# Kernel tuning notes

Measured on AMD Instinct MI355X. Metric: run time of the kernel, lower is better.

The kernel has to match this reference:

```python
import jax, jax.numpy as jnp
import numpy as np

N = 100000                       # all_nodes_num
COUNTS = (40000, 30000, 30000)   # node_type_split_list; type 0 is the attributed type
HID = 64                         # args.hidden_dim
K = 8                            # args.cluster_num
E = 1_600_000                    # number of edges in g
D_IN = 512                       # in_dims[valid_attributed_type]
NCLS = 16                        # num_classes


def _spmm_mean(h, src, dst):
    """Degree-normalized sparse adjacency @ h via gather/segment_sum (edge-list spmm)."""
    deg = jax.ops.segment_sum(jnp.ones_like(src, dtype=h.dtype), dst, num_segments=N)
    agg = jax.ops.segment_sum(h[src], dst, num_segments=N)  # [N, HID]
    return agg / jnp.maximum(deg, 1.0)[:, None]


def setup_inputs() -> dict:
    key = jax.random.key(0)
    ks = jax.random.split(key, 16)
    s = lambda k, shp, fan: jax.random.normal(k, shp, jnp.float32) * np.float32(1.0 / np.sqrt(fan))
    return {
        "feats0": jax.random.normal(ks[0], (COUNTS[0], D_IN), jnp.float32),
        "W_pre": s(ks[1], (D_IN, HID), D_IN), "b_pre": jnp.zeros((HID,), jnp.float32),
        "emb_W": s(ks[2], (2, COUNTS[1], HID), COUNTS[1]), "emb_b": jnp.zeros((2, HID), jnp.float32),
        "op_W": s(ks[3], (K, HID, HID), HID), "op_b": jnp.zeros((K, HID), jnp.float32),
        "fc_W": s(ks[4], (2, HID, HID), HID), "fc_b": jnp.zeros((2, HID), jnp.float32),
        "gnn_W": s(ks[5], (HID, HID), HID), "gnn_b": jnp.zeros((HID,), jnp.float32),
        "out_W": s(ks[6], (HID, NCLS), HID), "out_b": jnp.zeros((NCLS,), jnp.float32),
        "src": jax.random.randint(ks[7], (E,), 0, N, jnp.int32),
        "dst": jax.random.randint(ks[8], (E,), 0, N, jnp.int32),
        "node_assign": jax.random.randint(ks[9], (N,), 0, K, jnp.int32),
    }


def reference(feats0, W_pre, b_pre, emb_W, emb_b, op_W, op_b, fc_W, fc_b,
              gnn_W, gnn_b, out_W, out_b, src, dst, node_assign):
    # preprocess: Linear on the attributed type, scattered into h0 over all nodes
    h_attr = feats0 @ W_pre + b_pre                       # [n0, HID]
    h0 = jnp.zeros((N, HID), feats0.dtype).at[:COUNTS[0]].set(h_attr)

    # 'one-hot' embeddings: Linear applied to sparse identity == weight rows + bias
    one_hot_h = jnp.concatenate([
        jnp.zeros((COUNTS[0], HID), feats0.dtype),
        emb_W[0] + emb_b[0],
        emb_W[1] + emb_b[1],
    ], axis=0)                                            # [N, HID]

    # shared heterogeneous-graph aggregation (edge-list spmm), per-cluster op linear,
    # then diagonal cluster mask (spmm with diagonal selection matrix == row masking)
    agg = _spmm_mean(h0, src, dst)                        # [N, HID]
    h_att = h0
    for k in range(K):
        mask = (node_assign == k)[:, None]
        gcn_k = agg @ op_W[k] + op_b[k]                   # per-cluster GNN op output
        h_att = h_att + jnp.where(mask, gcn_k + one_hot_h, 0.0)

    # useTypeLinear: per-type Linear for non-attributed types, identity for attributed
    parts = [h_att[:COUNTS[0]]]
    off = COUNTS[0]
    for i in range(2):
        seg = h_att[off:off + COUNTS[1 + i]]
        parts.append(seg @ fc_W[i] + fc_b[i])
        off += COUNTS[1 + i]
    h_t = jnp.concatenate(parts, axis=0)                  # [N, HID]

    # downstream GCN-style model: spmm -> linear -> elu, then classifier head
    node_emb = jax.nn.elu(_spmm_mean(h_t, src, dst) @ gnn_W + gnn_b)
    logits = node_emb @ out_W + out_b
    return node_emb, logits, logits
```

## Files before the change

kernel.cpp:

```cpp
#include <hip/hip_runtime.h>
#include <hip/hip_bf16.h>

#define NN   100000
#define C0   40000
#define C1   30000
#define C2   30000
#define HID  64
#define KK   8
#define EE   1600000
#define DIN  512
#define NCLS 16
#define NB   196
#define BKE  2048
#define GR1  782
#define PMB  625
#define NBC  1568
#define SCH  7
#define MAXT 1571
#define FCT  469
#define GNT  1563
#define AP   88

typedef unsigned short ushortT;
typedef __attribute__((ext_vector_type(8))) short bf16x8;
typedef __attribute__((ext_vector_type(4))) float f32x4;

__device__ __forceinline__ float b2f(ushortT u) {
    return __uint_as_float((unsigned)u << 16);
}
__device__ __forceinline__ ushortT f2b(float x) {
    unsigned v = __float_as_uint(x);
    unsigned r = (v + 0x7FFF + ((v >> 16) & 1)) >> 16;
    return (ushortT)r;
}
__device__ __forceinline__ unsigned pk2(float lo, float hi) {
    return (unsigned)f2b(lo) | ((unsigned)f2b(hi) << 16);
}
__device__ __forceinline__ void acc8f(float* a, uint4 v) {
    a[0] += b2f((ushortT)(v.x & 0xFFFF)); a[1] += b2f((ushortT)(v.x >> 16));
    a[2] += b2f((ushortT)(v.y & 0xFFFF)); a[3] += b2f((ushortT)(v.y >> 16));
    a[4] += b2f((ushortT)(v.z & 0xFFFF)); a[5] += b2f((ushortT)(v.z >> 16));
    a[6] += b2f((ushortT)(v.w & 0xFFFF)); a[7] += b2f((ushortT)(v.w >> 16));
}

__global__ __launch_bounds__(256) void zero_wt(const float* __restrict__ W,
                                               ushortT* __restrict__ WT,
                                               int* __restrict__ bcnt) {
    const int t = threadIdx.x, b = blockIdx.x;
    if (b < 16) {
        int idx = b * 256 + t;
        int c = idx >> 6, k8 = (idx & 63) * 8;
        uint4 v;
        v.x = pk2(W[(size_t)(k8 + 0) * HID + c], W[(size_t)(k8 + 1) * HID + c]);
        v.y = pk2(W[(size_t)(k8 + 2) * HID + c], W[(size_t)(k8 + 3) * HID + c]);
        v.z = pk2(W[(size_t)(k8 + 4) * HID + c], W[(size_t)(k8 + 5) * HID + c]);
        v.w = pk2(W[(size_t)(k8 + 6) * HID + c], W[(size_t)(k8 + 7) * HID + c]);
        *(uint4*)(WT + (size_t)c * DIN + k8) = v;
    } else {
        if (t < NB) bcnt[t] = 0;
    }
}

__global__ __launch_bounds__(256) void fused_a(const float* __restrict__ A,
                                               const ushortT* __restrict__ WT,
                                               const float* __restrict__ bias,
                                               const int* __restrict__ dst,
                                               const int* __restrict__ na,
                                               int* __restrict__ bcnt,
                                               int* __restrict__ nbc,
                                               ushortT* __restrict__ hb) {
    __shared__ ushortT Ak[2][64 * AP];
    __shared__ ushortT Bk[2][64 * AP];
    const int tid = threadIdx.x, b = blockIdx.x;
    if (b < PMB) {
        const int row0 = b * 64;
        const int rr = tid >> 2, q = tid & 3;
        const int w = tid >> 6, l = tid & 63;
        const int lr = l & 15, g = l >> 4;
        f32x4 acc[4] = {{0.f,0.f,0.f,0.f},{0.f,0.f,0.f,0.f},{0.f,0.f,0.f,0.f},{0.f,0.f,0.f,0.f}};
        float4 av0, av1, av2, av3;
        uint4 bv0, bv1;
        {
            const float* ap = A + (size_t)(row0 + rr) * DIN + q * 16;
            av0 = *(const float4*)(ap + 0);  av1 = *(const float4*)(ap + 4);
            av2 = *(const float4*)(ap + 8);  av3 = *(const float4*)(ap + 12);
            const uint4* bp = (const uint4*)(WT + (size_t)rr * DIN + q * 16);
            bv0 = bp[0]; bv1 = bp[1];
        }
        {
            uint4 ua0, ua1;
            ua0.x = pk2(av0.x, av0.y); ua0.y = pk2(av0.z, av0.w);
            ua0.z = pk2(av1.x, av1.y); ua0.w = pk2(av1.z, av1.w);
            ua1.x = pk2(av2.x, av2.y); ua1.y = pk2(av2.z, av2.w);
            ua1.z = pk2(av3.x, av3.y); ua1.w = pk2(av3.z, av3.w);
            *(uint4*)&Ak[0][rr * AP + q * 16] = ua0;
            *(uint4*)&Ak[0][rr * AP + q * 16 + 8] = ua1;
            *(uint4*)&Bk[0][rr * AP + q * 16] = bv0;
            *(uint4*)&Bk[0][rr * AP + q * 16 + 8] = bv1;
        }
        __syncthreads();
        for (int tt = 0; tt < 8; ++tt) {
            if (tt < 7) {
                const int k0 = (tt + 1) * 64;
                const float* ap = A + (size_t)(row0 + rr) * DIN + k0 + q * 16;
                av0 = *(const float4*)(ap + 0);  av1 = *(const float4*)(ap + 4);
                av2 = *(const float4*)(ap + 8);  av3 = *(const float4*)(ap + 12);
                const uint4* bp = (const uint4*)(WT + (size_t)rr * DIN + k0 + q * 16);
                bv0 = bp[0]; bv1 = bp[1];
            }
            const int bu = tt & 1;
            #pragma unroll
            for (int s = 0; s < 2; ++s) {
                bf16x8 af = *(const bf16x8*)&Ak[bu][(w * 16 + lr) * AP + s * 32 + g * 8];
                #pragma unroll
                for (int n = 0; n < 4; ++n) {
                    bf16x8 bf = *(const bf16x8*)&Bk[bu][(n * 16 + lr) * AP + s * 32 + g * 8];
                    acc[n] = __builtin_amdgcn_mfma_f32_16x16x32_bf16(af, bf, acc[n], 0, 0, 0);
                }
            }
            if (tt < 7) {
                const int nb2 = (tt + 1) & 1;
                uint4 ua0, ua1;
                ua0.x = pk2(av0.x, av0.y); ua0.y = pk2(av0.z, av0.w);
                ua0.z = pk2(av1.x, av1.y); ua0.w = pk2(av1.z, av1.w);
                ua1.x = pk2(av2.x, av2.y); ua1.y = pk2(av2.z, av2.w);
                ua1.z = pk2(av3.x, av3.y); ua1.w = pk2(av3.z, av3.w);
                *(uint4*)&Ak[nb2][rr * AP + q * 16] = ua0;
                *(uint4*)&Ak[nb2][rr * AP + q * 16 + 8] = ua1;
                *(uint4*)&Bk[nb2][rr * AP + q * 16] = bv0;
                *(uint4*)&Bk[nb2][rr * AP + q * 16 + 8] = bv1;
            }
            __syncthreads();
        }
        #pragma unroll
        for (int n = 0; n < 4; ++n) {
            float bb = bias[n * 16 + lr];
            #pragma unroll
            for (int i = 0; i < 4; ++i) {
                int row = row0 + w * 16 + g * 4 + i;
                hb[(size_t)row * HID + n * 16 + lr] = f2b(acc[n][i] + bb);
            }
        }
    } else if (b < PMB + GR1) {
        int* sh = (int*)&Ak[0][0];
        for (int i = tid; i < NB; i += 256) sh[i] = 0;
        __syncthreads();
        const int base = (b - PMB) * BKE;
        for (int u = 0; u < BKE / 256; ++u) {
            int e = base + tid + u * 256;
            if (e < EE) atomicAdd(&sh[dst[e] >> 9], 1);
        }
        __syncthreads();
        for (int i = tid; i < NB; i += 256) {
            int c = sh[i];
            if (c) atomicAdd(&bcnt[i], c);
        }
    } else {
        int* sh = (int*)&Ak[0][0];
        const int nb_ = b - PMB - GR1;
        if (tid < KK) sh[tid] = 0;
        __syncthreads();
        #pragma unroll
        for (int u = 0; u < 2; ++u) {
            int n = nb_ * 512 + tid + u * 256;
            if (n < NN) atomicAdd(&sh[na[n]], 1);
        }
        __syncthreads();
        if (tid < KK) nbc[tid * NB + nb_] = sh[tid];
    }
}

__global__ __launch_bounds__(256) void scan_k(const int* __restrict__ bcnt,
                                              int* __restrict__ bbase,
                                              int* __restrict__ bcur,
                                              int* __restrict__ offs,
                                              const int* __restrict__ nbc,
                                              int* __restrict__ gbase,
                                              int* __restrict__ koff,
                                              int* __restrict__ tmap_b,
                                              int* __restrict__ tmap_s) {
    __shared__ int sm[256];
    const int t = threadIdx.x;
    if (blockIdx.x == 0) {
        int v = (t < NB) ? bcnt[t] : 0;
        sm[t] = v;
        __syncthreads();
        for (int off = 1; off < 256; off <<= 1) {
            int y = (t >= off) ? sm[t - off] : 0;
            __syncthreads();
            sm[t] += y;
            __syncthreads();
        }
        if (t < NB) {
            int excl = sm[t] - v;
            bbase[t] = excl;
            bcur[t] = excl;
        }
        if (t == 0) offs[NN] = EE;
        return;
    }
    __shared__ int carry;
    __shared__ int tl[KK];
    if (t == 0) carry = 0;
    for (int i = t; i < MAXT; i += 256) tmap_b[i] = -1;
    __syncthreads();
    for (int c = 0; c < SCH; ++c) {
        int i = c * 256 + t;
        int v = (i < NBC) ? nbc[i] : 0;
        sm[t] = v;
        __syncthreads();
        for (int off = 1; off < 256; off <<= 1) {
            int y = (t >= off) ? sm[t - off] : 0;
            __syncthreads();
            sm[t] += y;
            __syncthreads();
        }
        int base = carry;
        int excl = base + sm[t] - v;
        if (i < NBC) {
            gbase[i] = excl;
            if ((i % NB) == 0) koff[i / NB] = excl;
        }
        __syncthreads();
        if (t == 255) carry = base + sm[255];
        __syncthreads();
    }
    if (t == 0) {
        koff[KK] = NN;
        int run = 0;
        for (int k = 0; k < KK; ++k) {
            tl[k] = run;
            int cnt = ((k == KK - 1) ? NN : koff[k + 1]) - koff[k];
            run += (cnt + 63) / 64;
        }
    }
    __syncthreads();
    if (t < KK) {
        int k = t;
        int kb = koff[k];
        int ke = (k == KK - 1) ? NN : koff[k + 1];
        int nt = (ke - kb + 63) / 64;
        for (int tt = 0; tt < nt; ++tt) {
            tmap_b[tl[k] + tt] = k;
            tmap_s[tl[k] + tt] = kb + tt * 64;
        }
    }
}

__global__ __launch_bounds__(256) void scatter_k(const int* __restrict__ src,
                                                 const int* __restrict__ dst,
                                                 int* __restrict__ bcur,
                                                 unsigned* __restrict__ ebuf,
                                                 const int* __restrict__ na,
                                                 const int* __restrict__ gbase,
                                                 int* __restrict__ perm) {
    __shared__ int s1[NB];
    __shared__ int s2[NB];
    const int t = threadIdx.x, b = blockIdx.x;
    if (b < GR1) {
        for (int i = t; i < NB; i += 256) s1[i] = 0;
        __syncthreads();
        const int base = b * BKE;
        unsigned mypk[8]; int mybin[8], myrank[8];
        #pragma unroll
        for (int u = 0; u < 8; ++u) {
            int e = base + t + u * 256;
            if (e < EE) {
                int d = dst[e];
                int s = src[e];
                mybin[u] = d >> 9;
                mypk[u] = (unsigned)s |
                          ((unsigned)(((d & 511) << 1) | (s < C0 ? 0 : 1)) << 17);
                myrank[u] = atomicAdd(&s1[mybin[u]], 1);
            } else mybin[u] = -1;
        }
        __syncthreads();
        for (int i = t; i < NB; i += 256) {
            int c = s1[i];
            s2[i] = c ? atomicAdd(&bcur[i], c) : 0;
        }
        __syncthreads();
        #pragma unroll
        for (int u = 0; u < 8; ++u) {
            if (mybin[u] >= 0) {
                ebuf[s2[mybin[u]] + myrank[u]] = mypk[u];
            }
        }
    } else {
        const int nb_ = b - GR1;
        if (t < KK) { s1[t] = 0; s2[t] = gbase[t * NB + nb_]; }
        __syncthreads();
        #pragma unroll
        for (int u = 0; u < 2; ++u) {
            int n = nb_ * 512 + t + u * 256;
            if (n < NN) {
                int k = na[n];
                int r = atomicAdd(&s1[k], 1);
                perm[s2[k] + r] = n;
            }
        }
    }
}

__global__ __launch_bounds__(256) void fine_scatter(const unsigned* __restrict__ ebuf,
                                                    const int* __restrict__ bbase,
                                                    const int* __restrict__ bend,
                                                    int* __restrict__ offs,
                                                    int* __restrict__ split,
                                                    int* __restrict__ ssrc) {
    __shared__ int hist[1024];
    __shared__ int lofs[1024];
    __shared__ int sm[256];
    const int t = threadIdx.x, b = blockIdx.x;
    const int beg = bbase[b], end = bend[b];
    for (int i = t; i < 1024; i += 256) hist[i] = 0;
    __syncthreads();
    for (int j = beg + t; j < end; j += 256) {
        unsigned pk = ebuf[j];
        atomicAdd(&hist[pk >> 17], 1);
    }
    __syncthreads();
    int v0 = hist[4 * t], v1 = hist[4 * t + 1], v2 = hist[4 * t + 2], v3 = hist[4 * t + 3];
    int ts = v0 + v1 + v2 + v3;
    sm[t] = ts;
    __syncthreads();
    for (int off = 1; off < 256; off <<= 1) {
        int y = (t >= off) ? sm[t - off] : 0;
        __syncthreads();
        sm[t] += y;
        __syncthreads();
    }
    int pre = sm[t] - ts;
    lofs[4 * t] = pre; lofs[4 * t + 1] = pre + v0;
    lofs[4 * t + 2] = pre + v0 + v1; lofs[4 * t + 3] = pre + v0 + v1 + v2;
    __syncthreads();
    const int d0 = b * 512;
    for (int i = t; i < 512; i += 256) {
        int n = d0 + i;
        if (n < NN) {
            offs[n]  = beg + lofs[2 * i];
            split[n] = beg + lofs[2 * i + 1];
        }
    }
    __syncthreads();
    for (int j = beg + t; j < end; j += 256) {
        unsigned pk = ebuf[j];
        int pos = beg + atomicAdd(&lofs[pk >> 17], 1);
        ssrc[pos] = (int)(pk & 0x1FFFFu);
    }
}

__global__ __launch_bounds__(256) void spmm(const ushortT* __restrict__ rows,
                                            const int* __restrict__ offs,
                                            const int* __restrict__ splt,
                                            const int* __restrict__ ssrc,
                                            ushortT* __restrict__ aggb) {
    const int t = threadIdx.x;
    const int g = t >> 3, c8 = t & 7;
    const int n = blockIdx.x * 32 + g;
    const int beg = offs[n], endf = offs[n + 1];
    const int ge = splt ? splt[n] : endf;
    float a[8] = {}, c[8] = {};
    int j = beg;
    for (; j + 8 <= ge; j += 8) {
        int s0 = ssrc[j + 0], s1 = ssrc[j + 1], s2 = ssrc[j + 2], s3 = ssrc[j + 3];
        int s4 = ssrc[j + 4], s5 = ssrc[j + 5], s6 = ssrc[j + 6], s7 = ssrc[j + 7];
        uint4 v0 = *(const uint4*)(rows + (size_t)s0 * HID + c8 * 8);
        uint4 v1 = *(const uint4*)(rows + (size_t)s1 * HID + c8 * 8);
        uint4 v2 = *(const uint4*)(rows + (size_t)s2 * HID + c8 * 8);
        uint4 v3 = *(const uint4*)(rows + (size_t)s3 * HID + c8 * 8);
        uint4 v4 = *(const uint4*)(rows + (size_t)s4 * HID + c8 * 8);
        uint4 v5 = *(const uint4*)(rows + (size_t)s5 * HID + c8 * 8);
        uint4 v6 = *(const uint4*)(rows + (size_t)s6 * HID + c8 * 8);
        uint4 v7 = *(const uint4*)(rows + (size_t)s7 * HID + c8 * 8);
        acc8f(a, v0); acc8f(c, v1); acc8f(a, v2); acc8f(c, v3);
        acc8f(a, v4); acc8f(c, v5); acc8f(a, v6); acc8f(c, v7);
    }
    if (j + 4 <= ge) {
        int s0 = ssrc[j + 0], s1 = ssrc[j + 1], s2 = ssrc[j + 2], s3 = ssrc[j + 3];
        uint4 v0 = *(const uint4*)(rows + (size_t)s0 * HID + c8 * 8);
        uint4 v1 = *(const uint4*)(rows + (size_t)s1 * HID + c8 * 8);
        uint4 v2 = *(const uint4*)(rows + (size_t)s2 * HID + c8 * 8);
        uint4 v3 = *(const uint4*)(rows + (size_t)s3 * HID + c8 * 8);
        acc8f(a, v0); acc8f(c, v1); acc8f(a, v2); acc8f(c, v3);
        j += 4;
    }
    for (; j < ge; ++j) {
        uint4 v = *(const uint4*)(rows + (size_t)ssrc[j] * HID + c8 * 8);
        acc8f(a, v);
    }
    const float inv = 1.0f / fmaxf((float)(endf - beg), 1.0f);
    #pragma unroll
    for (int i = 0; i < 8; ++i) a[i] = (a[i] + c[i]) * inv;
    uint4 o;
    o.x = pk2(a[0], a[1]); o.y = pk2(a[2], a[3]);
    o.z = pk2(a[4], a[5]); o.w = pk2(a[6], a[7]);
    *(uint4*)(aggb + (size_t)n * HID + c8 * 8) = o;
}

__device__ __forceinline__ void gemm64(const float As[64][65], const float Bs[64][64],
                                       float acc[4][4], int tx, int ty) {
    for (int kk = 0; kk < 64; ++kk) {
        float a0 = As[ty * 4 + 0][kk], a1 = As[ty * 4 + 1][kk];
        float a2 = As[ty * 4 + 2][kk], a3 = As[ty * 4 + 3][kk];
        float4 bv = *(const float4*)(&Bs[kk][tx * 4]);
        acc[0][0] += a0 * bv.x; acc[0][1] += a0 * bv.y; acc[0][2] += a0 * bv.z; acc[0][3] += a0 * bv.w;
        acc[1][0] += a1 * bv.x; acc[1][1] += a1 * bv.y; acc[1][2] += a1 * bv.z; acc[1][3] += a1 * bv.w;
        acc[2][0] += a2 * bv.x; acc[2][1] += a2 * bv.y; acc[2][2] += a2 * bv.z; acc[2][3] += a2 * bv.w;
        acc[3][0] += a3 * bv.x; acc[3][1] += a3 * bv.y; acc[3][2] += a3 * bv.z; acc[3][3] += a3 * bv.w;
    }
}

__global__ __launch_bounds__(256) void op_gemm(const ushortT* __restrict__ aggb,
                                               const ushortT* __restrict__ hb,
                                               const int* __restrict__ perm,
                                               const int* __restrict__ koff,
                                               const int* __restrict__ tmap_b,
                                               const int* __restrict__ tmap_s,
                                               const float* __restrict__ op_W,
                                               const float* __restrict__ op_b,
                                               const float* __restrict__ emb_W,
                                               const float* __restrict__ emb_b,
                                               ushortT* __restrict__ htb) {
    __shared__ float As[64][65];
    __shared__ float Bs[64][64];
    __shared__ int idx[64];
    const int bk = tmap_b[blockIdx.x];
    if (bk < 0) return;
    const int start = tmap_s[blockIdx.x];
    const int kend = koff[bk + 1];
    const int tid = threadIdx.x;
    if (tid < 64) {
        int p = start + tid;
        idx[tid] = (p < kend) ? perm[p] : -1;
    }
    __syncthreads();
    for (int i = tid; i < 64 * 16; i += 256) {
        int r = i >> 4, c4 = i & 15;
        int n = idx[r];
        if (n >= 0) {
            ushort4 u = *(const ushort4*)(aggb + (size_t)n * HID + c4 * 4);
            As[r][c4 * 4 + 0] = b2f(u.x); As[r][c4 * 4 + 1] = b2f(u.y);
            As[r][c4 * 4 + 2] = b2f(u.z); As[r][c4 * 4 + 3] = b2f(u.w);
        } else {
            As[r][c4 * 4 + 0] = 0.f; As[r][c4 * 4 + 1] = 0.f;
            As[r][c4 * 4 + 2] = 0.f; As[r][c4 * 4 + 3] = 0.f;
        }
    }
    for (int i = tid; i < 64 * 16; i += 256) {
        int r = i >> 4, c4 = i & 15;
        *(float4*)(&Bs[r][c4 * 4]) = *(const float4*)(op_W + (size_t)bk * HID * HID + (size_t)r * HID + c4 * 4);
    }
    __syncthreads();
    const int tx = tid & 15, ty = tid >> 4;
    float acc[4][4] = {};
    gemm64(As, Bs, acc, tx, ty);
    float4 ob = *(const float4*)(op_b + (size_t)bk * HID + tx * 4);
    #pragma unroll
    for (int rr = 0; rr < 4; ++rr) {
        int n = idx[ty * 4 + rr];
        if (n < 0) continue;
        float4 v;
        v.x = acc[rr][0] + ob.x; v.y = acc[rr][1] + ob.y;
        v.z = acc[rr][2] + ob.z; v.w = acc[rr][3] + ob.w;
        if (n < C0) {
            ushort4 hu = *(const ushort4*)(hb + (size_t)n * HID + tx * 4);
            v.x += b2f(hu.x); v.y += b2f(hu.y); v.z += b2f(hu.z); v.w += b2f(hu.w);
        } else {
            int si = (n < C0 + C1) ? 0 : 1;
            int rn = n - C0 - si * C1;
            float4 ew = *(const float4*)(emb_W + ((size_t)si * C1 + rn) * HID + tx * 4);
            float4 eb = *(const float4*)(emb_b + (size_t)si * HID + tx * 4);
            v.x += ew.x + eb.x; v.y += ew.y + eb.y;
            v.z += ew.z + eb.z; v.w += ew.w + eb.w;
        }
        ushort4 o;
        o.x = f2b(v.x); o.y = f2b(v.y); o.z = f2b(v.z); o.w = f2b(v.w);
        *(ushort4*)(htb + (size_t)n * HID + tx * 4) = o;
    }
}

__global__ __launch_bounds__(256) void fc_gemm(ushortT* __restrict__ htb,
                                               const float* __restrict__ fc_W,
                                               const float* __restrict__ fc_b) {
    __shared__ float As[64][65];
    __shared__ float Bs[64][64];
    const int si = (blockIdx.x < FCT) ? 0 : 1;
    const int t0 = blockIdx.x - si * FCT;
    const int row0 = C0 + si * C1 + t0 * 64;
    const int lim = C0 + (si + 1) * C1;
    const int tid = threadIdx.x;
    for (int i = tid; i < 64 * 16; i += 256) {
        int r = i >> 4, c4 = i & 15;
        int n = row0 + r;
        if (n < lim) {
            ushort4 u = *(const ushort4*)(htb + (size_t)n * HID + c4 * 4);
            As[r][c4 * 4 + 0] = b2f(u.x); As[r][c4 * 4 + 1] = b2f(u.y);
            As[r][c4 * 4 + 2] = b2f(u.z); As[r][c4 * 4 + 3] = b2f(u.w);
        } else {
            As[r][c4 * 4 + 0] = 0.f; As[r][c4 * 4 + 1] = 0.f;
            As[r][c4 * 4 + 2] = 0.f; As[r][c4 * 4 + 3] = 0.f;
        }
    }
    for (int i = tid; i < 64 * 16; i += 256) {
        int r = i >> 4, c4 = i & 15;
        *(float4*)(&Bs[r][c4 * 4]) = *(const float4*)(fc_W + (size_t)si * HID * HID + (size_t)r * HID + c4 * 4);
    }
    __syncthreads();
    const int tx = tid & 15, ty = tid >> 4;
    float acc[4][4] = {};
    gemm64(As, Bs, acc, tx, ty);
    float4 fb = *(const float4*)(fc_b + (size_t)si * HID + tx * 4);
    #pragma unroll
    for (int rr = 0; rr < 4; ++rr) {
        int n = row0 + ty * 4 + rr;
        if (n >= lim) continue;
        ushort4 o;
        o.x = f2b(acc[rr][0] + fb.x); o.y = f2b(acc[rr][1] + fb.y);
        o.z = f2b(acc[rr][2] + fb.z); o.w = f2b(acc[rr][3] + fb.w);
        *(ushort4*)(htb + (size_t)n * HID + tx * 4) = o;
    }
}

__global__ __launch_bounds__(256) void gnn_logits(const ushortT* __restrict__ aggb,
                                                  const float* __restrict__ gnn_W,
                                                  const float* __restrict__ gnn_b,
                                                  const float* __restrict__ out_W,
                                                  const float* __restrict__ out_b,
                                                  float* __restrict__ out) {
    __shared__ float As[64][65];
    __shared__ float Bs[64][64];
    __shared__ float Wo[64 * NCLS];
    const int row0 = blockIdx.x * 64;
    const int tid = threadIdx.x;
    for (int i = tid; i < 64 * 16; i += 256) {
        int r = i >> 4, c4 = i & 15;
        int n = row0 + r;
        if (n < NN) {
            ushort4 u = *(const ushort4*)(aggb + (size_t)n * HID + c4 * 4);
            As[r][c4 * 4 + 0] = b2f(u.x); As[r][c4 * 4 + 1] = b2f(u.y);
            As[r][c4 * 4 + 2] = b2f(u.z); As[r][c4 * 4 + 3] = b2f(u.w);
        } else {
            As[r][c4 * 4 + 0] = 0.f; As[r][c4 * 4 + 1] = 0.f;
            As[r][c4 * 4 + 2] = 0.f; As[r][c4 * 4 + 3] = 0.f;
        }
    }
    for (int i = tid; i < 64 * 16; i += 256) {
        int r = i >> 4, c4 = i & 15;
        *(float4*)(&Bs[r][c4 * 4]) = *(const float4*)(gnn_W + (size_t)r * HID + c4 * 4);
    }
    *(float4*)(&Wo[tid * 4]) = *(const float4*)(out_W + tid * 4);
    __syncthreads();
    const int tx = tid & 15, ty = tid >> 4;
    float acc[4][4] = {};
    gemm64(As, Bs, acc, tx, ty);
    __syncthreads();
    float4 gb = *(const float4*)(gnn_b + tx * 4);
    #pragma unroll
    for (int rr = 0; rr < 4; ++rr) {
        int n = row0 + ty * 4 + rr;
        float4 v;
        v.x = acc[rr][0] + gb.x; v.y = acc[rr][1] + gb.y;
        v.z = acc[rr][2] + gb.z; v.w = acc[rr][3] + gb.w;
        v.x = (v.x > 0.f) ? v.x : expm1f(v.x);
        v.y = (v.y > 0.f) ? v.y : expm1f(v.y);
        v.z = (v.z > 0.f) ? v.z : expm1f(v.z);
        v.w = (v.w > 0.f) ? v.w : expm1f(v.w);
        As[ty * 4 + rr][tx * 4 + 0] = v.x; As[ty * 4 + rr][tx * 4 + 1] = v.y;
        As[ty * 4 + rr][tx * 4 + 2] = v.z; As[ty * 4 + rr][tx * 4 + 3] = v.w;
        if (n < NN) *(float4*)(out + (size_t)n * HID + tx * 4) = v;
    }
    __syncthreads();
    const int r = tid >> 2, cq = (tid & 3) * 4;
    float l0 = 0.f, l1 = 0.f, l2 = 0.f, l3 = 0.f;
    #pragma unroll 8
    for (int j = 0; j < 64; ++j) {
        float e = As[r][j];
        float4 w = *(const float4*)(&Wo[j * NCLS + cq]);
        l0 += e * w.x; l1 += e * w.y; l2 += e * w.z; l3 += e * w.w;
    }
    int n = row0 + r;
    if (n < NN) {
        float4 ob = *(const float4*)(out_b + cq);
        float4 lg;
        lg.x = l0 + ob.x; lg.y = l1 + ob.y; lg.z = l2 + ob.z; lg.w = l3 + ob.w;
        const size_t lbase = (size_t)NN * HID;
        *(float4*)(out + lbase + (size_t)n * NCLS + cq) = lg;
        *(float4*)(out + lbase + (size_t)NN * NCLS + (size_t)n * NCLS + cq) = lg;
    }
}

extern "C" void kernel_launch(void* const* d_in, const int* in_sizes, int n_in,
                              void* d_out, int out_size, void* d_ws, size_t ws_size,
                              hipStream_t stream) {
    const float* feats0 = (const float*)d_in[0];
    const float* W_pre  = (const float*)d_in[1];
    const float* b_pre  = (const float*)d_in[2];
    const float* emb_W  = (const float*)d_in[3];
    const float* emb_b  = (const float*)d_in[4];
    const float* op_W   = (const float*)d_in[5];
    const float* op_b   = (const float*)d_in[6];
    const float* fc_W   = (const float*)d_in[7];
    const float* fc_b   = (const float*)d_in[8];
    const float* gnn_W  = (const float*)d_in[9];
    const float* gnn_b  = (const float*)d_in[10];
    const float* out_W  = (const float*)d_in[11];
    const float* out_b  = (const float*)d_in[12];
    const int* src         = (const int*)d_in[13];
    const int* dst         = (const int*)d_in[14];
    const int* node_assign = (const int*)d_in[15];
    float* out = (float*)d_out;

    ushortT* hb  = (ushortT*)d_ws;
    ushortT* htb = hb + (size_t)C0 * HID;
    ushortT* aggb = htb + (size_t)NN * HID;
    unsigned* ebuf = (unsigned*)aggb;
    ushortT* WT = aggb + (size_t)NN * HID;
    int* ssrc   = (int*)(WT + (size_t)HID * DIN);
    int* offs   = ssrc + EE;
    int* split  = offs + NN + 1;
    int* perm   = split + NN;
    int* nbc    = perm + NN;
    int* gbase  = nbc + NBC;
    int* koff   = gbase + NBC;
    int* tmap_b = koff + KK + 1;
    int* tmap_s = tmap_b + MAXT;
    int* bcnt   = tmap_s + MAXT;
    int* bbase  = bcnt + NB;
    int* bcur   = bbase + NB;

    zero_wt<<<17, 256, 0, stream>>>(W_pre, WT, bcnt);
    fused_a<<<PMB + GR1 + NB, 256, 0, stream>>>(feats0, WT, b_pre, dst, node_assign,
                                                bcnt, nbc, hb);
    scan_k<<<2, 256, 0, stream>>>(bcnt, bbase, bcur, offs, nbc, gbase, koff, tmap_b, tmap_s);
    scatter_k<<<GR1 + NB, 256, 0, stream>>>(src, dst, bcur, ebuf, node_assign, gbase, perm);
    fine_scatter<<<NB, 256, 0, stream>>>(ebuf, bbase, bcur, offs, split, ssrc);
    spmm<<<NN / 32, 256, 0, stream>>>(hb, offs, split, ssrc, aggb);
    op_gemm<<<MAXT, 256, 0, stream>>>(aggb, hb, perm, koff, tmap_b, tmap_s,
                                      op_W, op_b, emb_W, emb_b, htb);
    fc_gemm<<<2 * FCT, 256, 0, stream>>>(htb, fc_W, fc_b);
    spmm<<<NN / 32, 256, 0, stream>>>(htb, offs, nullptr, ssrc, aggb);
    gnn_logits<<<GNT, 256, 0, stream>>>(aggb, gnn_W, gnn_b, out_W, out_b, out);
}
```

Baseline: 213.1 us.

## Replace scalar fp32 64x64 GEMM tiles with bf16 MFMA in three kernels

Swaps the shared-memory FP32 register-tiled GEMM used by op_gemm, fc_gemm and gnn_logits for bf16 MFMA 16x16x32 instructions. A tiles are staged in LDS as raw bf16 and weights are transposed and converted to bf16 per block. The aim is to cut ALU time and LDS footprint in the dense 64-wide projections. It costs weight precision (fp32 to bf16) and gives narrower per-element epilogue stores that coalesce less well than the old float4/ushort4 stores.

Result: faster. 195.7 us (-8.2%).

```diff
diff --git a/kernel.cpp b/kernel.cpp
--- a/kernel.cpp
+++ b/kernel.cpp
@@ -398,19 +398,6 @@
     *(uint4*)(aggb + (size_t)n * HID + c8 * 8) = o;
 }
 
-__device__ __forceinline__ void gemm64(const float As[64][65], const float Bs[64][64],
-                                       float acc[4][4], int tx, int ty) {
-    for (int kk = 0; kk < 64; ++kk) {
-        float a0 = As[ty * 4 + 0][kk], a1 = As[ty * 4 + 1][kk];
-        float a2 = As[ty * 4 + 2][kk], a3 = As[ty * 4 + 3][kk];
-        float4 bv = *(const float4*)(&Bs[kk][tx * 4]);
-        acc[0][0] += a0 * bv.x; acc[0][1] += a0 * bv.y; acc[0][2] += a0 * bv.z; acc[0][3] += a0 * bv.w;
-        acc[1][0] += a1 * bv.x; acc[1][1] += a1 * bv.y; acc[1][2] += a1 * bv.z; acc[1][3] += a1 * bv.w;
-        acc[2][0] += a2 * bv.x; acc[2][1] += a2 * bv.y; acc[2][2] += a2 * bv.z; acc[2][3] += a2 * bv.w;
-        acc[3][0] += a3 * bv.x; acc[3][1] += a3 * bv.y; acc[3][2] += a3 * bv.z; acc[3][3] += a3 * bv.w;
-    }
-}
-
 __global__ __launch_bounds__(256) void op_gemm(const ushortT* __restrict__ aggb,
                                                const ushortT* __restrict__ hb,
                                                const int* __restrict__ perm,
@@ -422,103 +409,122 @@
                                                const float* __restrict__ emb_W,
                                                const float* __restrict__ emb_b,
                                                ushortT* __restrict__ htb) {
-    __shared__ float As[64][65];
-    __shared__ float Bs[64][64];
+    __shared__ ushortT Ak[64 * AP];
+    __shared__ ushortT Bk[64 * AP];
     __shared__ int idx[64];
     const int bk = tmap_b[blockIdx.x];
     if (bk < 0) return;
     const int start = tmap_s[blockIdx.x];
     const int kend = koff[bk + 1];
     const int tid = threadIdx.x;
+    const int rr = tid >> 2, q = tid & 3;
     if (tid < 64) {
         int p = start + tid;
         idx[tid] = (p < kend) ? perm[p] : -1;
     }
     __syncthreads();
-    for (int i = tid; i < 64 * 16; i += 256) {
-        int r = i >> 4, c4 = i & 15;
-        int n = idx[r];
+    {
+        int n = idx[rr];
+        uint4 a0 = {0,0,0,0}, a1 = {0,0,0,0};
         if (n >= 0) {
-            ushort4 u = *(const ushort4*)(aggb + (size_t)n * HID + c4 * 4);
-            As[r][c4 * 4 + 0] = b2f(u.x); As[r][c4 * 4 + 1] = b2f(u.y);
-            As[r][c4 * 4 + 2] = b2f(u.z); As[r][c4 * 4 + 3] = b2f(u.w);
-        } else {
-            As[r][c4 * 4 + 0] = 0.f; As[r][c4 * 4 + 1] = 0.f;
-            As[r][c4 * 4 + 2] = 0.f; As[r][c4 * 4 + 3] = 0.f;
-        }
-    }
-    for (int i = tid; i < 64 * 16; i += 256) {
-        int r = i >> 4, c4 = i & 15;
-        *(float4*)(&Bs[r][c4 * 4]) = *(const float4*)(op_W + (size_t)bk * HID * HID + (size_t)r * HID + c4 * 4);
-    }
-    __syncthreads();
-    const int tx = tid & 15, ty = tid >> 4;
-    float acc[4][4] = {};
-    gemm64(As, Bs, acc, tx, ty);
-    float4 ob = *(const float4*)(op_b + (size_t)bk * HID + tx * 4);
+            const uint4* p = (const uint4*)(aggb + (size_t)n * HID + q * 16);
+            a0 = p[0]; a1 = p[1];
+        }
+        *(uint4*)&Ak[rr * AP + q * 16] = a0;
+        *(uint4*)&Ak[rr * AP + q * 16 + 8] = a1;
+    }
+    {
+        const float* wp = op_W + (size_t)bk * HID * HID;
+        #pragma unroll
+        for (int j = 0; j < 16; ++j) {
+            Bk[rr * AP + q * 16 + j] = f2b(wp[(size_t)(q * 16 + j) * HID + rr]);
+        }
+    }
+    __syncthreads();
+    const int w = tid >> 6, l = tid & 63;
+    const int lr = l & 15, g = l >> 4;
+    f32x4 acc[4] = {{0.f,0.f,0.f,0.f},{0.f,0.f,0.f,0.f},{0.f,0.f,0.f,0.f},{0.f,0.f,0.f,0.f}};
     #pragma unroll
-    for (int rr = 0; rr < 4; ++rr) {
-        int n = idx[ty * 4 + rr];
-        if (n < 0) continue;
-        float4 v;
-        v.x = acc[rr][0] + ob.x; v.y = acc[rr][1] + ob.y;
-        v.z = acc[rr][2] + ob.z; v.w = acc[rr][3] + ob.w;
-        if (n < C0) {
-            ushort4 hu = *(const ushort4*)(hb + (size_t)n * HID + tx * 4);
-            v.x += b2f(hu.x); v.y += b2f(hu.y); v.z += b2f(hu.z); v.w += b2f(hu.w);
-        } else {
-            int si = (n < C0 + C1) ? 0 : 1;
-            int rn = n - C0 - si * C1;
-            float4 ew = *(const float4*)(emb_W + ((size_t)si * C1 + rn) * HID + tx * 4);
-            float4 eb = *(const float4*)(emb_b + (size_t)si * HID + tx * 4);
-            v.x += ew.x + eb.x; v.y += ew.y + eb.y;
-            v.z += ew.z + eb.z; v.w += ew.w + eb.w;
-        }
-        ushort4 o;
-        o.x = f2b(v.x); o.y = f2b(v.y); o.z = f2b(v.z); o.w = f2b(v.w);
-        *(ushort4*)(htb + (size_t)n * HID + tx * 4) = o;
+    for (int s = 0; s < 2; ++s) {
+        bf16x8 af = *(const bf16x8*)&Ak[(w * 16 + lr) * AP + s * 32 + g * 8];
+        #pragma unroll
+        for (int n = 0; n < 4; ++n) {
+            bf16x8 bf = *(const bf16x8*)&Bk[(n * 16 + lr) * AP + s * 32 + g * 8];
+            acc[n] = __builtin_amdgcn_mfma_f32_16x16x32_bf16(af, bf, acc[n], 0, 0, 0);
+        }
+    }
+    #pragma unroll
+    for (int n = 0; n < 4; ++n) {
+        const int col = n * 16 + lr;
+        float ob = op_b[bk * HID + col];
+        #pragma unroll
+        for (int i = 0; i < 4; ++i) {
+            int node = idx[w * 16 + g * 4 + i];
+            if (node < 0) continue;
+            float v = acc[n][i] + ob;
+            if (node < C0) {
+                v += b2f(hb[(size_t)node * HID + col]);
+            } else {
+                int si = (node < C0 + C1) ? 0 : 1;
+                int rn = node - C0 - si * C1;
+                v += emb_W[((size_t)si * C1 + rn) * HID + col] + emb_b[si * HID + col];
+            }
+            htb[(size_t)node * HID + col] = f2b(v);
+        }
     }
 }
 
 __global__ __launch_bounds__(256) void fc_gemm(ushortT* __restrict__ htb,
                                                const float* __restrict__ fc_W,
                                                const float* __restrict__ fc_b) {
-    __shared__ float As[64][65];
-    __shared__ float Bs[64][64];
+    __shared__ ushortT Ak[64 * AP];
+    __shared__ ushortT Bk[64 * AP];
     const int si = (blockIdx.x < FCT) ? 0 : 1;
     const int t0 = blockIdx.x - si * FCT;
     const int row0 = C0 + si * C1 + t0 * 64;
     const int lim = C0 + (si + 1) * C1;
     const int tid = threadIdx.x;
-    for (int i = tid; i < 64 * 16; i += 256) {
-        int r = i >> 4, c4 = i & 15;
-        int n = row0 + r;
+    const int rr = tid >> 2, q = tid & 3;
+    {
+        int n = row0 + rr;
+        uint4 a0 = {0,0,0,0}, a1 = {0,0,0,0};
         if (n < lim) {
-            ushort4 u = *(const ushort4*)(htb + (size_t)n * HID + c4 * 4);
-            As[r][c4 * 4 + 0] = b2f(u.x); As[r][c4 * 4 + 1] = b2f(u.y);
-            As[r][c4 * 4 + 2] = b2f(u.z); As[r][c4 * 4 + 3] = b2f(u.w);
-        } else {
-            As[r][c4 * 4 + 0] = 0.f; As[r][c4 * 4 + 1] = 0.f;
-            As[r][c4 * 4 + 2] = 0.f; As[r][c4 * 4 + 3] = 0.f;
-        }
-    }
-    for (int i = tid; i < 64 * 16; i += 256) {
-        int r = i >> 4, c4 = i & 15;
-        *(float4*)(&Bs[r][c4 * 4]) = *(const float4*)(fc_W + (size_t)si * HID * HID + (size_t)r * HID + c4 * 4);
-    }
-    __syncthreads();
-    const int tx = tid & 15, ty = tid >> 4;
-    float acc[4][4] = {};
-    gemm64(As, Bs, acc, tx, ty);
-    float4 fb = *(const float4*)(fc_b + (size_t)si * HID + tx * 4);
+            const uint4* p = (const uint4*)(htb + (size_t)n * HID + q * 16);
+            a0 = p[0]; a1 = p[1];
+        }
+        *(uint4*)&Ak[rr * AP + q * 16] = a0;
+        *(uint4*)&Ak[rr * AP + q * 16 + 8] = a1;
+    }
+    {
+        const float* wp = fc_W + (size_t)si * HID * HID;
+        #pragma unroll
+        for (int j = 0; j < 16; ++j) {
+            Bk[rr * AP + q * 16 + j] = f2b(wp[(size_t)(q * 16 + j) * HID + rr]);
+        }
+    }
+    __syncthreads();
+    const int w = tid >> 6, l = tid & 63;
+    const int lr = l & 15, g = l >> 4;
+    f32x4 acc[4] = {{0.f,0.f,0.f,0.f},{0.f,0.f,0.f,0.f},{0.f,0.f,0.f,0.f},{0.f,0.f,0.f,0.f}};
     #pragma unroll
-    for (int rr = 0; rr < 4; ++rr) {
-        int n = row0 + ty * 4 + rr;
-        if (n >= lim) continue;
-        ushort4 o;
-        o.x = f2b(acc[rr][0] + fb.x); o.y = f2b(acc[rr][1] + fb.y);
-        o.z = f2b(acc[rr][2] + fb.z); o.w = f2b(acc[rr][3] + fb.w);
-        *(ushort4*)(htb + (size_t)n * HID + tx * 4) = o;
+    for (int s = 0; s < 2; ++s) {
+        bf16x8 af = *(const bf16x8*)&Ak[(w * 16 + lr) * AP + s * 32 + g * 8];
+        #pragma unroll
+        for (int n = 0; n < 4; ++n) {
+            bf16x8 bf = *(const bf16x8*)&Bk[(n * 16 + lr) * AP + s * 32 + g * 8];
+            acc[n] = __builtin_amdgcn_mfma_f32_16x16x32_bf16(af, bf, acc[n], 0, 0, 0);
+        }
+    }
+    #pragma unroll
+    for (int n = 0; n < 4; ++n) {
+        const int col = n * 16 + lr;
+        float fb = fc_b[si * HID + col];
+        #pragma unroll
+        for (int i = 0; i < 4; ++i) {
+            int node = row0 + w * 16 + g * 4 + i;
+            if (node >= lim) continue;
+            htb[(size_t)node * HID + col] = f2b(acc[n][i] + fb);
+        }
     }
 }
 
@@ -528,56 +534,65 @@
                                                   const float* __restrict__ out_W,
                                                   const float* __restrict__ out_b,
                                                   float* __restrict__ out) {
-    __shared__ float As[64][65];
-    __shared__ float Bs[64][64];
+    __shared__ ushortT Ak[64 * AP];
+    __shared__ ushortT Bk[64 * AP];
+    __shared__ float Em[64][65];
     __shared__ float Wo[64 * NCLS];
     const int row0 = blockIdx.x * 64;
     const int tid = threadIdx.x;
-    for (int i = tid; i < 64 * 16; i += 256) {
-        int r = i >> 4, c4 = i & 15;
-        int n = row0 + r;
+    const int rr = tid >> 2, q = tid & 3;
+    {
+        int n = row0 + rr;
+        uint4 a0 = {0,0,0,0}, a1 = {0,0,0,0};
         if (n < NN) {
-            ushort4 u = *(const ushort4*)(aggb + (size_t)n * HID + c4 * 4);
-            As[r][c4 * 4 + 0] = b2f(u.x); As[r][c4 * 4 + 1] = b2f(u.y);
-            As[r][c4 * 4 + 2] = b2f(u.z); As[r][c4 * 4 + 3] = b2f(u.w);
-        } else {
-            As[r][c4 * 4 + 0] = 0.f; As[r][c4 * 4 + 1] = 0.f;
-            As[r][c4 * 4 + 2] = 0.f; As[r][c4 * 4 + 3] = 0.f;
-        }
-    }
-    for (int i = tid; i < 64 * 16; i += 256) {
-        int r = i >> 4, c4 = i & 15;
-        *(float4*)(&Bs[r][c4 * 4]) = *(const float4*)(gnn_W + (size_t)r * HID + c4 * 4);
+            const uint4* p = (const uint4*)(aggb + (size_t)n * HID + q * 16);
+            a0 = p[0]; a1 = p[1];
+        }
+        *(uint4*)&Ak[rr * AP + q * 16] = a0;
+        *(uint4*)&Ak[rr * AP + q * 16 + 8] = a1;
+    }
+    {
+        #pragma unroll
+        for (int j = 0; j < 16; ++j) {
+            Bk[rr * AP + q * 16 + j] = f2b(gnn_W[(size_t)(q * 16 + j) * HID + rr]);
+        }
     }
     *(float4*)(&Wo[tid * 4]) = *(const float4*)(out_W + tid * 4);
     __syncthreads();
-    const int tx = tid & 15, ty = tid >> 4;
-    float acc[4][4] = {};
-    gemm64(As, Bs, acc, tx, ty);
-    __syncthreads();
-    float4 gb = *(const float4*)(gnn_b + tx * 4);
+    const int w = tid >> 6, l = tid & 63;
+    const int lr = l & 15, g = l >> 4;
+    f32x4 acc[4] = {{0.f,0.f,0.f,0.f},{0.f,0.f,0.f,0.f},{0.f,0.f,0.f,0.f},{0.f,0.f,0.f,0.f}};
     #pragma unroll
-    for (int rr = 0; rr < 4; ++rr) {
-        int n = row0 + ty * 4 + rr;
-        float4 v;
-        v.x = acc[rr][0] + gb.x; v.y = acc[rr][1] + gb.y;
-        v.z = acc[rr][2] + gb.z; v.w = acc[rr][3] + gb.w;
-        v.x = (v.x > 0.f) ? v.x : expm1f(v.x);
-        v.y = (v.y > 0.f) ? v.y : expm1f(v.y);
-        v.z = (v.z > 0.f) ? v.z : expm1f(v.z);
-        v.w = (v.w > 0.f) ? v.w : expm1f(v.w);
-        As[ty * 4 + rr][tx * 4 + 0] = v.x; As[ty * 4 + rr][tx * 4 + 1] = v.y;
-        As[ty * 4 + rr][tx * 4 + 2] = v.z; As[ty * 4 + rr][tx * 4 + 3] = v.w;
-        if (n < NN) *(float4*)(out + (size_t)n * HID + tx * 4) = v;
+    for (int s = 0; s < 2; ++s) {
+        bf16x8 af = *(const bf16x8*)&Ak[(w * 16 + lr) * AP + s * 32 + g * 8];
+        #pragma unroll
+        for (int n = 0; n < 4; ++n) {
+            bf16x8 bf = *(const bf16x8*)&Bk[(n * 16 + lr) * AP + s * 32 + g * 8];
+            acc[n] = __builtin_amdgcn_mfma_f32_16x16x32_bf16(af, bf, acc[n], 0, 0, 0);
+        }
+    }
+    #pragma unroll
+    for (int n = 0; n < 4; ++n) {
+        const int col = n * 16 + lr;
+        float gb = gnn_b[col];
+        #pragma unroll
+        for (int i = 0; i < 4; ++i) {
+            int lrow = w * 16 + g * 4 + i;
+            int node = row0 + lrow;
+            float v = acc[n][i] + gb;
+            v = (v > 0.f) ? v : expm1f(v);
+            Em[lrow][col] = v;
+            if (node < NN) out[(size_t)node * HID + col] = v;
+        }
     }
     __syncthreads();
     const int r = tid >> 2, cq = (tid & 3) * 4;
     float l0 = 0.f, l1 = 0.f, l2 = 0.f, l3 = 0.f;
     #pragma unroll 8
     for (int j = 0; j < 64; ++j) {
-        float e = As[r][j];
-        float4 w = *(const float4*)(&Wo[j * NCLS + cq]);
-        l0 += e * w.x; l1 += e * w.y; l2 += e * w.z; l3 += e * w.w;
+        float e = Em[r][j];
+        float4 wv = *(const float4*)(&Wo[j * NCLS + cq]);
+        l0 += e * wv.x; l1 += e * wv.y; l2 += e * wv.z; l3 += e * wv.w;
     }
     int n = row0 + r;
     if (n < NN) {
```
